# Optimization experiments

Measured on AMD Instinct MI355X. Metric: run time of the kernel, lower is better.

The kernel has to match this reference:

```python
import jax, jax.numpy as jnp
import numpy as np

N, F_IN, HID, C, H = 4096, 1024, 64, 40, 8
ALPHA = 0.2  # LeakyReLU negative slope
NEG_INF = -9e15

def setup_inputs() -> dict:
    key = jax.random.key(0)
    ks = jax.random.split(key, 8)
    x = jax.random.normal(ks[0], (N, F_IN), jnp.float32)
    adj = jax.random.randint(ks[1], (N, N), 0, 2, jnp.int32)  # dense 0/1 adjacency
    W = jax.random.normal(ks[2], (H, F_IN, HID), jnp.float32) / np.sqrt(F_IN).astype(np.float32)
    a_src = jax.random.normal(ks[3], (H, HID), jnp.float32) * 0.1
    a_dst = jax.random.normal(ks[4], (H, HID), jnp.float32) * 0.1
    W_out = jax.random.normal(ks[5], (H * HID, C), jnp.float32) / np.sqrt(H * HID).astype(np.float32)
    ao_src = jax.random.normal(ks[6], (C,), jnp.float32) * 0.1
    ao_dst = jax.random.normal(ks[7], (C,), jnp.float32) * 0.1
    return dict(x=x, adj=adj, W=W, a_src=a_src, a_dst=a_dst,
                W_out=W_out, ao_src=ao_src, ao_dst=ao_dst)

def _masked_attention(src, dst, mask):
    # src: [..., N] scores for row node i; dst: [..., N] scores for col node j
    e = jax.nn.leaky_relu(src[..., :, None] + dst[..., None, :], ALPHA)  # [..., N, N]
    e = jnp.where(mask, e, NEG_INF)
    return jax.nn.softmax(e, axis=-1)

def reference(x, adj, W, a_src, a_dst, W_out, ao_src, ao_dst):
    mask = adj > 0  # [N, N]
    # multi-head GAT layer (concat=True)
    Wh = jnp.einsum('nf,hfo->hno', x, W)            # [H, N, HID]
    src = jnp.einsum('hno,ho->hn', Wh, a_src)       # [H, N]
    dst = jnp.einsum('hno,ho->hn', Wh, a_dst)       # [H, N]
    att = _masked_attention(src, dst, mask[None])   # [H, N, N]
    h = jnp.einsum('hij,hjo->hio', att, Wh)         # [H, N, HID]
    h = jax.nn.elu(h)                               # concat=True -> elu inside layer
    h = jnp.transpose(h, (1, 0, 2)).reshape(N, H * HID)  # concat heads -> [N, H*HID]
    # output GAT layer (concat=False -> no elu inside)
    Wh2 = h @ W_out                                 # [N, C]
    att2 = _masked_attention(Wh2 @ ao_src, Wh2 @ ao_dst, mask)  # [N, N]
    out = att2 @ Wh2                                # [N, C]
    # model-level: elu then log_softmax over classes
    return jax.nn.log_softmax(jax.nn.elu(out), axis=1)
```

## Files before the change

### kernel.cpp

```cpp
#include <hip/hip_runtime.h>

#define NN 4096
#define F_IN 1024
#define NHEAD 8
#define HID 64
#define NCLS 40
#define LOG2E 1.44269504f

typedef float f32x4 __attribute__((ext_vector_type(4)));
typedef float f32x2 __attribute__((ext_vector_type(2)));
typedef short s16x8 __attribute__((ext_vector_type(8)));

#define SWZ(r,c) (((r)*64) + ((c) ^ (((r)&7)<<3)))

__device__ __forceinline__ unsigned short f2bf(float f){
  unsigned u = __float_as_uint(f);
  return (unsigned short)((u + 0x7fffu + ((u >> 16) & 1u)) >> 16);
}
__device__ __forceinline__ unsigned cvtpk(float lo, float hi){
  unsigned r; asm("v_cvt_pk_bf16_f32 %0, %1, %2" : "=v"(r) : "v"(lo), "v"(hi)); return r;
}
__device__ __forceinline__ f32x2 pkmul(f32x2 a, f32x2 b){
  f32x2 r; asm("v_pk_mul_f32 %0, %1, %2" : "=v"(r) : "v"(a), "v"(b)); return r;
}

__global__ __launch_bounds__(256) void pack_adj_k(const int* __restrict__ adj, unsigned* __restrict__ bmT){
  int gid = blockIdx.x*256 + threadIdx.x;
  int lane = threadIdx.x & 63;
  unsigned long long m = __ballot(adj[gid] > 0);
  int w = gid >> 5, i = w >> 7, jw = w & 127;
  if (lane == 0)       bmT[(size_t)jw*NN + i] = (unsigned)m;
  else if (lane == 32) bmT[(size_t)jw*NN + i] = (unsigned)(m >> 32);
}

__global__ __launch_bounds__(256) void cast_W_k(const float* __restrict__ W, unsigned short* __restrict__ WbT){
  __shared__ float T[64][65];
  const int h = blockIdx.y, k0 = blockIdx.x*64, t = threadIdx.x;
  for (int idx = t; idx < 1024; idx += 256){
    int k = idx >> 4, c4 = idx & 15;
    *(float4*)&T[k][c4*4] = *(const float4*)&W[((size_t)h*F_IN + k0 + k)*HID + c4*4];
  }
  __syncthreads();
  for (int idx = t; idx < 512; idx += 256){
    int o = idx >> 3, ch = idx & 7;
    s16x8 v;
    #pragma unroll
    for (int e = 0; e < 8; ++e) v[e] = (short)f2bf(T[ch*8 + e][o]);
    *(s16x8*)&WbT[((size_t)h*HID + o)*F_IN + k0 + ch*8] = v;
  }
}

__global__ __launch_bounds__(256) void cast_Wo_k(const float* __restrict__ Wout, unsigned short* __restrict__ WoT){
  int idx = blockIdx.x*256 + threadIdx.x;
  int cc = idx >> 9, k = idx & 511;
  WoT[idx] = (cc < NCLS) ? f2bf(Wout[(size_t)k*NCLS + cc]) : (unsigned short)0;
}

__global__ __launch_bounds__(256) void gemm1_k(const float* __restrict__ x,
    const unsigned short* __restrict__ WbT, unsigned short* __restrict__ WhT,
    const float* __restrict__ a_src, const float* __restrict__ a_dst,
    float* __restrict__ srcv, float* __restrict__ dstv, float2* __restrict__ bdv){
  __shared__ unsigned short xS[64*64];
  __shared__ unsigned short wS[64*64];
  const int t = threadIdx.x, l = t & 63, wv = t >> 6, g = l >> 4, c = l & 15;
  const int h = blockIdx.y, n0 = blockIdx.x * 64;
  f32x4 acc[4] = {};
  for (int k0 = 0; k0 < F_IN; k0 += 64){
    __syncthreads();
    #pragma unroll
    for (int p = 0; p < 4; ++p){
      int idx = t + p*256, row = idx >> 4, c4 = idx & 15;
      float4 v = *(const float4*)&x[(size_t)(n0+row)*F_IN + k0 + c4*4];
      *(uint2*)&xS[SWZ(row, c4*4)] = make_uint2(cvtpk(v.x, v.y), cvtpk(v.z, v.w));
    }
    #pragma unroll
    for (int p = 0; p < 2; ++p){
      int idx = t + p*256, o = idx >> 3, ch = idx & 7;
      *(s16x8*)&wS[SWZ(o, ch*8)] = *(const s16x8*)&WbT[(size_t)(h*HID + o)*F_IN + k0 + ch*8];
    }
    __syncthreads();
    #pragma unroll
    for (int ks = 0; ks < 2; ++ks){
      s16x8 av = *(const s16x8*)&xS[SWZ(wv*16 + c, ks*32 + g*8)];
      #pragma unroll
      for (int ct = 0; ct < 4; ++ct){
        s16x8 bv = *(const s16x8*)&wS[SWZ(ct*16 + c, ks*32 + g*8)];
        acc[ct] = __builtin_amdgcn_mfma_f32_16x16x32_bf16(av, bv, acc[ct], 0, 0, 0);
      }
    }
  }
  float asv[4], adv[4];
  #pragma unroll
  for (int ct = 0; ct < 4; ++ct){ asv[ct] = a_src[h*HID + ct*16 + c]; adv[ct] = a_dst[h*HID + ct*16 + c]; }
  #pragma unroll
  for (int r = 0; r < 4; ++r){
    float ps = acc[0][r]*asv[0] + acc[1][r]*asv[1] + acc[2][r]*asv[2] + acc[3][r]*asv[3];
    float pd = acc[0][r]*adv[0] + acc[1][r]*adv[1] + acc[2][r]*adv[2] + acc[3][r]*adv[3];
    #pragma unroll
    for (int off = 1; off < 16; off <<= 1){ ps += __shfl_xor(ps, off); pd += __shfl_xor(pd, off); }
    if (c == 0){
      int n = n0 + wv*16 + g*4 + r;
      srcv[h*NN + n] = ps; dstv[h*NN + n] = pd;
      bdv[h*NN + n] = make_float2(exp2f(pd*LOG2E), exp2f(0.2f*pd*LOG2E));
    }
  }
  __syncthreads();
  #pragma unroll
  for (int ct = 0; ct < 4; ++ct)
    *(uint2*)&xS[SWZ(ct*16 + c, wv*16 + g*4)] = make_uint2(cvtpk(acc[ct][0], acc[ct][1]), cvtpk(acc[ct][2], acc[ct][3]));
  __syncthreads();
  #pragma unroll
  for (int p = 0; p < 2; ++p){
    int idx = t + p*256, o = idx >> 3, ch = idx & 7;
    *(s16x8*)&WhT[(size_t)(h*HID + o)*NN + n0 + ch*8] = *(const s16x8*)&xS[SWZ(o, ch*8)];
  }
}

__global__ __launch_bounds__(256) void maxred_k(const float* __restrict__ in, float* __restrict__ out){
  __shared__ float red[4];
  const float* p = in + (size_t)blockIdx.x*NN;
  float m = -3.0e38f;
  for (int i = threadIdx.x; i < NN; i += 256) m = fmaxf(m, p[i]);
  #pragma unroll
  for (int off = 32; off; off >>= 1) m = fmaxf(m, __shfl_xor(m, off));
  if ((threadIdx.x & 63) == 0) red[threadIdx.x >> 6] = m;
  __syncthreads();
  if (threadIdx.x == 0) out[blockIdx.x] = fmaxf(fmaxf(red[0], red[1]), fmaxf(red[2], red[3]));
}

template<int NCT, int NJT, bool CHUNKED, bool DO_ELU>
__global__ __launch_bounds__(256) void agg_mfma_k(
    const unsigned* __restrict__ bmT, const unsigned short* __restrict__ VT,
    const float* __restrict__ srcv, const float2* __restrict__ bdv,
    const float* __restrict__ maxp, void* __restrict__ outp)
{
  __shared__ unsigned short vS[2][2][NCT*16*64];
  const int t = threadIdx.x, l = t & 63, wv = t >> 6, g = l >> 4, c = l & 15;
  const int h   = CHUNKED ? 0 : blockIdx.y;
  const int jt0 = CHUNKED ? blockIdx.y * NJT : 0;
  const int i0 = blockIdx.x * 32;
  const int tl = wv >> 1, rH = wv & 1;
  const int lr = rH*16 + c;
  const float sr = srcv[h*NN + i0 + lr];
  const float mx = maxp[CHUNKED ? 0 : h];
  const float tm = sr + mx;
  const float mi2 = fmaxf(tm, 0.2f*tm) * LOG2E;
  f32x2 ac2;
  ac2[0] = exp2f(fmaf(sr, LOG2E, -mi2));
  ac2[1] = exp2f(fmaf(0.2f*sr, LOG2E, -mi2));
  const unsigned short* vb = VT + (CHUNKED ? (size_t)0 : (size_t)h*HID*NN);
  const float2* bp = bdv + (CHUNKED ? (size_t)0 : (size_t)h*NN);

  f32x4 acc[NCT] = {};
  f32x4 accs = {};
  s16x8 ones;
  #pragma unroll
  for (int e = 0; e < 8; ++e) ones[e] = (short)0x3F80;

  s16x8 vreg[NCT];
  auto loadRegs = [&](int jt){
    #pragma unroll
    for (int p = 0; p < NCT; ++p){
      int u = t + p*256;
      int tt = u / (NCT*128), rem = u % (NCT*128);
      int o = rem >> 3, chk = rem & 7;
      vreg[p] = *(const s16x8*)&vb[(size_t)o*NN + (jt+tt)*64 + chk*8];
    }
  };
  auto writeLDS = [&](int b){
    #pragma unroll
    for (int p = 0; p < NCT; ++p){
      int u = t + p*256;
      int tt = u / (NCT*128), rem = u % (NCT*128);
      int o = rem >> 3, chk = rem & 7;
      *(s16x8*)&vS[b][tt][SWZ(o, chk*8)] = vreg[p];
    }
  };
  auto computeBuf = [&](int b, int jtile){
    unsigned wbit[2];
    wbit[0] = bmT[(size_t)(jtile*2 + 0)*NN + i0 + lr];
    wbit[1] = bmT[(size_t)(jtile*2 + 1)*NN + i0 + lr];
    #pragma unroll
    for (int ks = 0; ks < 2; ++ks){
      f32x2 drv[8];
      #pragma unroll
      for (int e = 0; e < 8; ++e) drv[e] = *(const f32x2*)&bp[jtile*64 + ks*32 + g*8 + e];
      s16x8 bv[NCT];
      #pragma unroll
      for (int ct = 0; ct < NCT; ++ct)
        bv[ct] = *(const s16x8*)&vS[b][tl][SWZ(ct*16 + c, ks*32 + g*8)];
      unsigned wb = (wbit[ks] >> (g*8)) & 0xffu;
      float q[8];
      #pragma unroll
      for (int e = 0; e < 8; ++e){
        f32x2 pr = pkmul(ac2, drv[e]);
        float m3 = __builtin_amdgcn_fmed3f(pr[0], pr[1], 1.0f);
        q[e] = (wb & (1u << e)) ? m3 : 0.f;
      }
      s16x8 afr;
      ((unsigned*)&afr)[0] = cvtpk(q[0], q[1]);
      ((unsigned*)&afr)[1] = cvtpk(q[2], q[3]);
      ((unsigned*)&afr)[2] = cvtpk(q[4], q[5]);
      ((unsigned*)&afr)[3] = cvtpk(q[6], q[7]);
      #pragma unroll
      for (int ct = 0; ct < NCT; ++ct)
        acc[ct] = __builtin_amdgcn_mfma_f32_16x16x32_bf16(afr, bv[ct], acc[ct], 0, 0, 0);
      accs = __builtin_amdgcn_mfma_f32_16x16x32_bf16(afr, ones, accs, 0, 0, 0);
    }
  };

  loadRegs(jt0);
  writeLDS(0);
  __syncthreads();
  int cur = 0;
  for (int jj = 0; jj < NJT; jj += 2){
    const bool more = (jj + 2 < NJT);
    if (more) loadRegs(jt0 + jj + 2);
    computeBuf(cur, jt0 + jj + tl);
    if (more) writeLDS(cur ^ 1);
    __syncthreads();
    cur ^= 1;
  }

  float* mrg = (float*)&vS[0][0][0];
  constexpr int S = (NCT + 1) * 4;
  if (tl == 1){
    int base = (rH*64 + l) * S;
    #pragma unroll
    for (int ct = 0; ct < NCT; ++ct)
      #pragma unroll
      for (int r = 0; r < 4; ++r) mrg[base + ct*4 + r] = acc[ct][r];
    #pragma unroll
    for (int r = 0; r < 4; ++r) mrg[base + NCT*4 + r] = accs[r];
  }
  __syncthreads();
  if (tl == 0){
    int base = (rH*64 + l) * S;
    #pragma unroll
    for (int ct = 0; ct < NCT; ++ct)
      #pragma unroll
      for (int r = 0; r < 4; ++r) acc[ct][r] += mrg[base + ct*4 + r];
    #pragma unroll
    for (int r = 0; r < 4; ++r) accs[r] += mrg[base + NCT*4 + r];
    if (!CHUNKED){
      unsigned short* ob = (unsigned short*)outp;
      #pragma unroll
      for (int r = 0; r < 4; ++r){
        float inv = 1.f / fmaxf(accs[r], 1e-30f);
        int row = i0 + rH*16 + g*4 + r;
        #pragma unroll
        for (int ct = 0; ct < NCT; ++ct){
          float v = acc[ct][r] * inv;
          if (DO_ELU) v = v > 0.f ? v : __expf(v) - 1.f;
          ob[(size_t)row*(NHEAD*HID) + h*HID + ct*16 + c] = f2bf(v);
        }
      }
    } else {
      float* ob = (float*)outp + (size_t)blockIdx.y * NN * 64;
      #pragma unroll
      for (int r = 0; r < 4; ++r){
        int row = i0 + rH*16 + g*4 + r;
        #pragma unroll
        for (int ct = 0; ct < NCT; ++ct)
          ob[(size_t)row*64 + ct*16 + c] = acc[ct][r];
        if (c == 0) ob[(size_t)row*64 + 48] = accs[r];
      }
    }
  }
}

__global__ __launch_bounds__(256) void gemm2_k(const unsigned short* __restrict__ hb,
    const unsigned short* __restrict__ WoT, const float* __restrict__ aos, const float* __restrict__ aod,
    unsigned short* __restrict__ WhT2, float* __restrict__ s2, float* __restrict__ d2,
    float2* __restrict__ bd2){
  __shared__ unsigned short aS[64*64];
  __shared__ unsigned short bS[48*64];
  const int t = threadIdx.x, l = t & 63, wv = t >> 6, g = l >> 4, c = l & 15;
  const int n0 = blockIdx.x * 64;
  f32x4 acc[3] = {};
  for (int k0 = 0; k0 < NHEAD*HID; k0 += 64){
    __syncthreads();
    #pragma unroll
    for (int p = 0; p < 2; ++p){
      int u = t + p*256, o = u >> 3, ch = u & 7;
      *(s16x8*)&aS[SWZ(o, ch*8)] = *(const s16x8*)&hb[(size_t)(n0+o)*(NHEAD*HID) + k0 + ch*8];
    }
    for (int u = t; u < 384; u += 256){
      int o = u >> 3, ch = u & 7;
      *(s16x8*)&bS[SWZ(o, ch*8)] = *(const s16x8*)&WoT[(size_t)o*(NHEAD*HID) + k0 + ch*8];
    }
    __syncthreads();
    #pragma unroll
    for (int ks = 0; ks < 2; ++ks){
      s16x8 av = *(const s16x8*)&aS[SWZ(wv*16 + c, ks*32 + g*8)];
      #pragma unroll
      for (int ct = 0; ct < 3; ++ct){
        s16x8 bv = *(const s16x8*)&bS[SWZ(ct*16 + c, ks*32 + g*8)];
        acc[ct] = __builtin_amdgcn_mfma_f32_16x16x32_bf16(av, bv, acc[ct], 0, 0, 0);
      }
    }
  }
  float asv[3], adv[3];
  #pragma unroll
  for (int ct = 0; ct < 3; ++ct){
    int col = ct*16 + c;
    asv[ct] = (col < NCLS) ? aos[col] : 0.f;
    adv[ct] = (col < NCLS) ? aod[col] : 0.f;
  }
  #pragma unroll
  for (int r = 0; r < 4; ++r){
    float ps = acc[0][r]*asv[0] + acc[1][r]*asv[1] + acc[2][r]*asv[2];
    float pd = acc[0][r]*adv[0] + acc[1][r]*adv[1] + acc[2][r]*adv[2];
    #pragma unroll
    for (int off = 1; off < 16; off <<= 1){ ps += __shfl_xor(ps, off); pd += __shfl_xor(pd, off); }
    if (c == 0){
      int n = n0 + wv*16 + g*4 + r;
      s2[n] = ps; d2[n] = pd;
      bd2[n] = make_float2(exp2f(pd*LOG2E), exp2f(0.2f*pd*LOG2E));
    }
  }
  __syncthreads();
  #pragma unroll
  for (int ct = 0; ct < 3; ++ct)
    *(uint2*)&bS[SWZ(ct*16 + c, wv*16 + g*4)] = make_uint2(cvtpk(acc[ct][0], acc[ct][1]), cvtpk(acc[ct][2], acc[ct][3]));
  __syncthreads();
  for (int u = t; u < 384; u += 256){
    int o = u >> 3, ch = u & 7;
    *(s16x8*)&WhT2[(size_t)o*NN + n0 + ch*8] = *(const s16x8*)&bS[SWZ(o, ch*8)];
  }
}

__global__ __launch_bounds__(256) void final_k(const float* __restrict__ part, float* __restrict__ out){
  const int wid = (blockIdx.x*256 + threadIdx.x) >> 6;
  const int c = threadIdx.x & 63;
  float acc = 0.f, rs = 0.f;
  #pragma unroll
  for (int ch = 0; ch < 8; ++ch){
    const float* pb = part + ((size_t)ch*NN + wid)*64;
    if (c < 48) acc += pb[c];
    rs += pb[48];
  }
  float v = acc / fmaxf(rs, 1e-30f);
  float e = v > 0.f ? v : __expf(v) - 1.f;
  float ev = (c < NCLS) ? e : -3.0e38f;
  float m = ev;
  #pragma unroll
  for (int off = 32; off; off >>= 1) m = fmaxf(m, __shfl_xor(m, off));
  float ex = (c < NCLS) ? __expf(e - m) : 0.f;
  float s = ex;
  #pragma unroll
  for (int off = 32; off; off >>= 1) s += __shfl_xor(s, off);
  if (c < NCLS) out[(size_t)wid*NCLS + c] = e - m - __logf(s);
}

extern "C" void kernel_launch(void* const* d_in, const int* in_sizes, int n_in,
                              void* d_out, int out_size, void* d_ws, size_t ws_size,
                              hipStream_t stream){
  (void)in_sizes; (void)n_in; (void)out_size; (void)ws_size;
  const float* x     = (const float*)d_in[0];
  const int*   adj   = (const int*)  d_in[1];
  const float* W     = (const float*)d_in[2];
  const float* a_src = (const float*)d_in[3];
  const float* a_dst = (const float*)d_in[4];
  const float* W_out = (const float*)d_in[5];
  const float* aos   = (const float*)d_in[6];
  const float* aod   = (const float*)d_in[7];
  float* out = (float*)d_out;

  char* p = (char*)d_ws;
  unsigned* bmT        = (unsigned*)p;       p += (size_t)NN*128*4;
  unsigned short* WbT  = (unsigned short*)p; p += (size_t)NHEAD*HID*F_IN*2;
  unsigned short* WhT  = (unsigned short*)p; p += (size_t)NHEAD*HID*NN*2;
  unsigned short* hbuf = (unsigned short*)p; p += (size_t)NN*NHEAD*HID*2;
  unsigned short* WoT  = (unsigned short*)p; p += (size_t)48*NHEAD*HID*2;
  unsigned short* WhT2 = (unsigned short*)p; p += (size_t)48*NN*2;
  float* srcv = (float*)p; p += (size_t)NHEAD*NN*4;
  float* dstv = (float*)p; p += (size_t)NHEAD*NN*4;
  float* maxd = (float*)p; p += 256;
  float* s2   = (float*)p; p += (size_t)NN*4;
  float* d2   = (float*)p; p += (size_t)NN*4;
  float* m2   = (float*)p; p += 256;
  float2* bdv1 = (float2*)p; p += (size_t)NHEAD*NN*8;
  float2* bdv2 = (float2*)p; p += (size_t)NN*8;
  float* part = (float*)p; p += (size_t)8*NN*64*4;

  pack_adj_k<<<(NN*NN)/256, 256, 0, stream>>>(adj, bmT);
  cast_W_k<<<dim3(F_IN/64, NHEAD), 256, 0, stream>>>(W, WbT);
  cast_Wo_k<<<96, 256, 0, stream>>>(W_out, WoT);
  gemm1_k<<<dim3(NN/64, NHEAD), 256, 0, stream>>>(x, WbT, WhT, a_src, a_dst, srcv, dstv, bdv1);
  maxred_k<<<NHEAD, 256, 0, stream>>>(dstv, maxd);
  agg_mfma_k<4, 64, false, true><<<dim3(NN/32, NHEAD), 256, 0, stream>>>(bmT, WhT, srcv, bdv1, maxd, hbuf);
  gemm2_k<<<NN/64, 256, 0, stream>>>(hbuf, WoT, aos, aod, WhT2, s2, d2, bdv2);
  maxred_k<<<1, 256, 0, stream>>>(d2, m2);
  agg_mfma_k<3, 8, true, false><<<dim3(NN/32, 8), 256, 0, stream>>>(bmT, WhT2, s2, bdv2, m2, part);
  final_k<<<NN/4, 256, 0, stream>>>(part, out);
}
```

Before: 163.3 us.

## Split layer-1 aggregation over two j-chunks and stage dst/mask bits in LDS

The first-layer attention aggregation is now split into two column chunks per head, which doubles the grid, and a new merge kernel sums the partial numerators and denominators, normalizes, applies ELU and casts to bf16. Separately, the per-tile dst scores and adjacency bit words are now prefetched into double-buffered shared memory alongside the V tiles, replacing per-lane global loads inside the compute loop. The aim is more parallelism and lower global-load latency in the inner loop. The cost is an extra kernel launch plus fp32 partial-sum traffic of about 16 MB written and read back.

```diff
diff --git a/kernel.cpp b/kernel.cpp
--- a/kernel.cpp
+++ b/kernel.cpp
@@ -128,28 +128,31 @@
   if (threadIdx.x == 0) out[blockIdx.x] = fmaxf(fmaxf(red[0], red[1]), fmaxf(red[2], red[3]));
 }
 
-template<int NCT, int NJT, bool CHUNKED, bool DO_ELU>
+template<int NCT, int NJT, int MODE>
 __global__ __launch_bounds__(256) void agg_mfma_k(
     const unsigned* __restrict__ bmT, const unsigned short* __restrict__ VT,
     const float* __restrict__ srcv, const float2* __restrict__ bdv,
-    const float* __restrict__ maxp, void* __restrict__ outp)
+    const float* __restrict__ maxp, float* __restrict__ partOut, float* __restrict__ denOut)
 {
   __shared__ unsigned short vS[2][2][NCT*16*64];
+  __shared__ float2 dS[2][2][64];
+  __shared__ unsigned bitS[2][2][2][32];
   const int t = threadIdx.x, l = t & 63, wv = t >> 6, g = l >> 4, c = l & 15;
-  const int h   = CHUNKED ? 0 : blockIdx.y;
-  const int jt0 = CHUNKED ? blockIdx.y * NJT : 0;
+  const int h  = (MODE == 0) ? (blockIdx.y >> 1) : 0;
+  const int ck = (MODE == 0) ? (blockIdx.y & 1)  : blockIdx.y;
+  const int jt0 = ck * NJT;
   const int i0 = blockIdx.x * 32;
   const int tl = wv >> 1, rH = wv & 1;
   const int lr = rH*16 + c;
   const float sr = srcv[h*NN + i0 + lr];
-  const float mx = maxp[CHUNKED ? 0 : h];
+  const float mx = maxp[MODE == 0 ? h : 0];
   const float tm = sr + mx;
   const float mi2 = fmaxf(tm, 0.2f*tm) * LOG2E;
   f32x2 ac2;
   ac2[0] = exp2f(fmaf(sr, LOG2E, -mi2));
   ac2[1] = exp2f(fmaf(0.2f*sr, LOG2E, -mi2));
-  const unsigned short* vb = VT + (CHUNKED ? (size_t)0 : (size_t)h*HID*NN);
-  const float2* bp = bdv + (CHUNKED ? (size_t)0 : (size_t)h*NN);
+  const unsigned short* vb = VT + (MODE == 0 ? (size_t)h*HID*NN : (size_t)0);
+  const float2* bp = bdv + (MODE == 0 ? (size_t)h*NN : (size_t)0);
 
   f32x4 acc[NCT] = {};
   f32x4 accs = {};
@@ -157,7 +160,7 @@
   #pragma unroll
   for (int e = 0; e < 8; ++e) ones[e] = (short)0x3F80;
 
-  s16x8 vreg[NCT];
+  s16x8 vreg[NCT]; float2 dreg = make_float2(0.f, 0.f); unsigned breg = 0;
   auto loadRegs = [&](int jt){
     #pragma unroll
     for (int p = 0; p < NCT; ++p){
@@ -166,6 +169,11 @@
       int o = rem >> 3, chk = rem & 7;
       vreg[p] = *(const s16x8*)&vb[(size_t)o*NN + (jt+tt)*64 + chk*8];
     }
+    if (t < 128){
+      f32x2 bd = *(const f32x2*)&bp[(jt + (t>>6))*64 + (t&63)];
+      dreg = make_float2(bd[0], bd[1]);
+    }
+    else { int u = t - 128; breg = bmT[(size_t)((jt + (u>>6))*2 + ((u>>5)&1))*NN + i0 + (u&31)]; }
   };
   auto writeLDS = [&](int b){
     #pragma unroll
@@ -175,25 +183,18 @@
       int o = rem >> 3, chk = rem & 7;
       *(s16x8*)&vS[b][tt][SWZ(o, chk*8)] = vreg[p];
     }
+    if (t < 128) dS[b][t>>6][t&63] = dreg;
+    else { int u = t - 128; bitS[b][u>>6][(u>>5)&1][u&31] = breg; }
   };
-  auto computeBuf = [&](int b, int jtile){
-    unsigned wbit[2];
-    wbit[0] = bmT[(size_t)(jtile*2 + 0)*NN + i0 + lr];
-    wbit[1] = bmT[(size_t)(jtile*2 + 1)*NN + i0 + lr];
+  auto computeBuf = [&](int b){
     #pragma unroll
     for (int ks = 0; ks < 2; ++ks){
-      f32x2 drv[8];
-      #pragma unroll
-      for (int e = 0; e < 8; ++e) drv[e] = *(const f32x2*)&bp[jtile*64 + ks*32 + g*8 + e];
-      s16x8 bv[NCT];
-      #pragma unroll
-      for (int ct = 0; ct < NCT; ++ct)
-        bv[ct] = *(const s16x8*)&vS[b][tl][SWZ(ct*16 + c, ks*32 + g*8)];
-      unsigned wb = (wbit[ks] >> (g*8)) & 0xffu;
+      unsigned wb = (bitS[b][tl][ks][lr] >> (g*8)) & 0xffu;
+      const f32x2* dr = (const f32x2*)&dS[b][tl][ks*32 + g*8];
       float q[8];
       #pragma unroll
       for (int e = 0; e < 8; ++e){
-        f32x2 pr = pkmul(ac2, drv[e]);
+        f32x2 pr = pkmul(ac2, dr[e]);
         float m3 = __builtin_amdgcn_fmed3f(pr[0], pr[1], 1.0f);
         q[e] = (wb & (1u << e)) ? m3 : 0.f;
       }
@@ -203,8 +204,10 @@
       ((unsigned*)&afr)[2] = cvtpk(q[4], q[5]);
       ((unsigned*)&afr)[3] = cvtpk(q[6], q[7]);
       #pragma unroll
-      for (int ct = 0; ct < NCT; ++ct)
-        acc[ct] = __builtin_amdgcn_mfma_f32_16x16x32_bf16(afr, bv[ct], acc[ct], 0, 0, 0);
+      for (int ct = 0; ct < NCT; ++ct){
+        s16x8 bv = *(const s16x8*)&vS[b][tl][SWZ(ct*16 + c, ks*32 + g*8)];
+        acc[ct] = __builtin_amdgcn_mfma_f32_16x16x32_bf16(afr, bv, acc[ct], 0, 0, 0);
+      }
       accs = __builtin_amdgcn_mfma_f32_16x16x32_bf16(afr, ones, accs, 0, 0, 0);
     }
   };
@@ -216,7 +219,7 @@
   for (int jj = 0; jj < NJT; jj += 2){
     const bool more = (jj + 2 < NJT);
     if (more) loadRegs(jt0 + jj + 2);
-    computeBuf(cur, jt0 + jj + tl);
+    computeBuf(cur);
     if (more) writeLDS(cur ^ 1);
     __syncthreads();
     cur ^= 1;
@@ -242,21 +245,18 @@
       for (int r = 0; r < 4; ++r) acc[ct][r] += mrg[base + ct*4 + r];
     #pragma unroll
     for (int r = 0; r < 4; ++r) accs[r] += mrg[base + NCT*4 + r];
-    if (!CHUNKED){
-      unsigned short* ob = (unsigned short*)outp;
+    if (MODE == 0){
+      float* ob = partOut + (size_t)ck * NN * (NHEAD*HID);
       #pragma unroll
       for (int r = 0; r < 4; ++r){
-        float inv = 1.f / fmaxf(accs[r], 1e-30f);
         int row = i0 + rH*16 + g*4 + r;
         #pragma unroll
-        for (int ct = 0; ct < NCT; ++ct){
-          float v = acc[ct][r] * inv;
-          if (DO_ELU) v = v > 0.f ? v : __expf(v) - 1.f;
-          ob[(size_t)row*(NHEAD*HID) + h*HID + ct*16 + c] = f2bf(v);
-        }
+        for (int ct = 0; ct < NCT; ++ct)
+          ob[(size_t)row*(NHEAD*HID) + h*HID + ct*16 + c] = acc[ct][r];
+        if (c == 0) denOut[(size_t)(ck*NHEAD + h)*NN + row] = accs[r];
       }
     } else {
-      float* ob = (float*)outp + (size_t)blockIdx.y * NN * 64;
+      float* ob = partOut + (size_t)ck * NN * 64;
       #pragma unroll
       for (int r = 0; r < 4; ++r){
         int row = i0 + rH*16 + g*4 + r;
@@ -267,6 +267,23 @@
       }
     }
   }
+}
+
+__global__ __launch_bounds__(256) void merge1_k(const float* __restrict__ part, const float* __restrict__ den,
+                                                unsigned short* __restrict__ hb){
+  int idx = blockIdx.x*256 + threadIdx.x;
+  int row = idx >> 7, q = idx & 127;
+  float4 a = *(const float4*)&part[(size_t)row*(NHEAD*HID) + q*4];
+  float4 b = *(const float4*)&part[((size_t)NN + row)*(NHEAD*HID) + q*4];
+  int h = q >> 4;
+  float dn = den[(size_t)h*NN + row] + den[(size_t)(NHEAD + h)*NN + row];
+  float inv = 1.f / fmaxf(dn, 1e-30f);
+  float v0 = (a.x + b.x)*inv, v1 = (a.y + b.y)*inv, v2 = (a.z + b.z)*inv, v3 = (a.w + b.w)*inv;
+  v0 = v0 > 0.f ? v0 : __expf(v0) - 1.f;
+  v1 = v1 > 0.f ? v1 : __expf(v1) - 1.f;
+  v2 = v2 > 0.f ? v2 : __expf(v2) - 1.f;
+  v3 = v3 > 0.f ? v3 : __expf(v3) - 1.f;
+  *(uint2*)&hb[(size_t)row*(NHEAD*HID) + q*4] = make_uint2(cvtpk(v0, v1), cvtpk(v2, v3));
 }
 
 __global__ __launch_bounds__(256) void gemm2_k(const unsigned short* __restrict__ hb,
@@ -382,16 +399,18 @@
   float* m2   = (float*)p; p += 256;
   float2* bdv1 = (float2*)p; p += (size_t)NHEAD*NN*8;
   float2* bdv2 = (float2*)p; p += (size_t)NN*8;
-  float* part = (float*)p; p += (size_t)8*NN*64*4;
+  float* den1 = (float*)p; p += (size_t)2*NHEAD*NN*4;
+  float* partU = (float*)p; p += (size_t)2*NN*NHEAD*HID*4;
 
   pack_adj_k<<<(NN*NN)/256, 256, 0, stream>>>(adj, bmT);
   cast_W_k<<<dim3(F_IN/64, NHEAD), 256, 0, stream>>>(W, WbT);
   cast_Wo_k<<<96, 256, 0, stream>>>(W_out, WoT);
   gemm1_k<<<dim3(NN/64, NHEAD), 256, 0, stream>>>(x, WbT, WhT, a_src, a_dst, srcv, dstv, bdv1);
   maxred_k<<<NHEAD, 256, 0, stream>>>(dstv, maxd);
-  agg_mfma_k<4, 64, false, true><<<dim3(NN/32, NHEAD), 256, 0, stream>>>(bmT, WhT, srcv, bdv1, maxd, hbuf);
+  agg_mfma_k<4, 32, 0><<<dim3(NN/32, 16), 256, 0, stream>>>(bmT, WhT, srcv, bdv1, maxd, partU, den1);
+  merge1_k<<<(NN*128)/256, 256, 0, stream>>>(partU, den1, hbuf);
   gemm2_k<<<NN/64, 256, 0, stream>>>(hbuf, WoT, aos, aod, WhT2, s2, d2, bdv2);
   maxred_k<<<1, 256, 0, stream>>>(d2, m2);
-  agg_mfma_k<3, 8, true, false><<<dim3(NN/32, 8), 256, 0, stream>>>(bmT, WhT2, s2, bdv2, m2, part);
-  final_k<<<NN/4, 256, 0, stream>>>(part, out);
-}
+  agg_mfma_k<3, 8, 1><<<dim3(NN/32, 8), 256, 0, stream>>>(bmT, WhT2, s2, bdv2, m2, partU, nullptr);
+  final_k<<<NN/4, 256, 0, stream>>>(partU, out);
+}
```

Result: no change. 162.0 us (-0.8%).
